# Kernel tuning notes

Measured on AMD Instinct MI355X. Metric: run time of the kernel, lower is better.

## Reference

```python
import jax, jax.numpy as jnp
import numpy as np

N = 50000
E = 800000
DIM_IN, DIM_H, DIM_OUT, HEADS = 128, 8, 32, 15
NEG_SLOPE = 0.2  # PyG GATv2Conv default


def gatv2_layer(x, src, dst, Wl, Wr, att, bias, num_nodes):
    """PyG GATv2Conv (share_weights=False, concat=True) with self-loops already in src/dst.
    x: [N, F_in]; Wl/Wr: [F_in, H*C]; att: [H, C]; bias: [H*C].
    """
    H, C = att.shape
    xl = (x @ Wl).reshape(-1, H, C)  # source transform [N,H,C]
    xr = (x @ Wr).reshape(-1, H, C)  # target transform [N,H,C]
    s = jax.nn.leaky_relu(xl[src] + xr[dst], negative_slope=NEG_SLOPE)  # [E,H,C]
    e = jnp.einsum('ehc,hc->eh', s, att)  # attention logits [E,H]
    # numerically-stable segment softmax over incoming edges of each dst node
    emax = jax.ops.segment_max(e, dst, num_segments=num_nodes)  # [N,H]
    ee = jnp.exp(e - emax[dst])
    denom = jax.ops.segment_sum(ee, dst, num_segments=num_nodes)  # [N,H]
    alpha = ee / denom[dst]  # self-loops guarantee denom > 0
    out = jax.ops.segment_sum(alpha[:, :, None] * xl[src], dst, num_segments=num_nodes)  # [N,H,C]
    return out.reshape(num_nodes, H * C) + bias


def setup_inputs() -> dict:
    key = jax.random.key(0)
    ks = jax.random.split(key, 10)
    x = jax.random.normal(ks[0], (N, DIM_IN), dtype=jnp.float32)
    edge_index = jax.random.randint(ks[1], (2, E), 0, N, dtype=jnp.int64)
    g1 = 1.0 / np.sqrt(DIM_IN)
    g2 = 1.0 / np.sqrt(DIM_H * HEADS)
    return {
        'x': x,
        'edge_index': edge_index,
        'W1l': jax.random.normal(ks[2], (DIM_IN, HEADS * DIM_H), dtype=jnp.float32) * g1,
        'W1r': jax.random.normal(ks[3], (DIM_IN, HEADS * DIM_H), dtype=jnp.float32) * g1,
        'att1': jax.random.normal(ks[4], (HEADS, DIM_H), dtype=jnp.float32) * (1.0 / np.sqrt(DIM_H)),
        'b1': jnp.zeros((HEADS * DIM_H,), dtype=jnp.float32),
        'W2l': jax.random.normal(ks[5], (HEADS * DIM_H, DIM_OUT), dtype=jnp.float32) * g2,
        'W2r': jax.random.normal(ks[6], (HEADS * DIM_H, DIM_OUT), dtype=jnp.float32) * g2,
        'att2': jax.random.normal(ks[7], (1, DIM_OUT), dtype=jnp.float32) * (1.0 / np.sqrt(DIM_OUT)),
        'b2': jnp.zeros((DIM_OUT,), dtype=jnp.float32),
    }


def reference(x, edge_index, W1l, W1r, att1, b1, W2l, W2r, att2, b2):
    n = x.shape[0]
    loops = jnp.arange(n, dtype=edge_index.dtype)
    src = jnp.concatenate([edge_index[0], loops])  # PyG add_self_loops=True
    dst = jnp.concatenate([edge_index[1], loops])
    h = gatv2_layer(x, src, dst, W1l, W1r, att1, b1, n)  # [N, HEADS*DIM_H]
    h = jax.nn.elu(h)
    # dropout(p=0.3) is identity in eval mode
    h = gatv2_layer(h, src, dst, W2l, W2r, att2, b2, n)  # heads=1 -> [N, DIM_OUT]
    return h, jax.nn.log_softmax(h, axis=1)
```

## Files before the change

### kernel.cpp

```cpp
#include <hip/hip_runtime.h>
#include <math.h>

namespace {
constexpr int NN  = 50000;
constexpr int EE  = 800000;
constexpr int FIN = 128;
constexpr int HC1 = 120;
constexpr int PAD = 128;
constexpr int F2  = 32;
constexpr int MT  = NN / 16;
constexpr int CAP = 64;
constexpr int NBIN = 64;
constexpr int BINW = 782;
constexpr int BINCAP = 16384;
constexpr int TILE = 4096;
constexpr int ABLK = (EE + TILE - 1) / TILE;
constexpr int CHUNKW = 12500;
constexpr int GB16 = (MT + 15) / 16;
constexpr int GB = (MT + 3) / 4;
constexpr float LOG2E = 1.442695041f;
}

typedef __attribute__((ext_vector_type(8))) short bf16x8;
typedef __attribute__((ext_vector_type(4))) float f32x4;
typedef __attribute__((ext_vector_type(2))) float f32x2;

template<int CTRL>
__device__ __forceinline__ float dppf(float x) {
    return __int_as_float(__builtin_amdgcn_mov_dpp(__float_as_int(x), CTRL, 0xF, 0xF, true));
}
__device__ __forceinline__ float quad_sum(float x) {
    x += dppf<0xB1>(x);
    x += dppf<0x4E>(x);
    return x;
}
__device__ __forceinline__ float rsum16(float x) {
    x += dppf<0x121>(x);
    x += dppf<0x122>(x);
    x += dppf<0x124>(x);
    x += dppf<0x128>(x);
    return x;
}
__device__ __forceinline__ float rmax16(float x) {
    x = fmaxf(x, dppf<0x121>(x));
    x = fmaxf(x, dppf<0x122>(x));
    x = fmaxf(x, dppf<0x124>(x));
    x = fmaxf(x, dppf<0x128>(x));
    return x;
}
template<int MASK>
__device__ __forceinline__ float swz_add(float x) {
    return x + __int_as_float(__builtin_amdgcn_ds_swizzle(__float_as_int(x), (MASK << 10) | 0x1F));
}

__device__ __forceinline__ unsigned short f2bf(float f) {
    unsigned int u = __float_as_uint(f);
    unsigned int r = (u + 0x7fffu + ((u >> 16) & 1u)) >> 16;
    return (unsigned short)r;
}
__device__ __forceinline__ f32x2 bf2v(unsigned int u) {
    f32x2 r;
    r.x = __uint_as_float(u << 16);
    r.y = __uint_as_float(u & 0xffff0000u);
    return r;
}
__device__ __forceinline__ f32x2 leaky2(f32x2 t) {
    return __builtin_elementwise_max(t, t * 0.2f);
}


__device__ void binA_body(int b, const unsigned int* __restrict__ raw,
                          int* __restrict__ cursor, unsigned int* __restrict__ binbuf) {
    __shared__ int lcnt[NBIN];
    __shared__ int lbase[NBIN];
    __shared__ int lcnt2[NBIN];
    __shared__ int is64_s;
    int tid = threadIdx.x;
    if (tid < NBIN) { lcnt[tid] = 0; lcnt2[tid] = 0; }
    if (tid < 64) {
        unsigned int hi = raw[2 * tid + 1];
        unsigned long long ball = __ballot(hi == 0u);
        if (tid == 0) is64_s = (ball == ~0ULL) ? 1 : 0;
    }
    __syncthreads();
    int is64 = is64_s;
    int e0 = b * TILE;
    #pragma unroll
    for (int i = 0; i < TILE / 256; ++i) {
        int e = e0 + i * 256 + tid;
        if (e < EE) {
            int d = is64 ? (int)raw[2 * (size_t)(EE + e)] : (int)raw[EE + e];
            atomicAdd(&lcnt[d / BINW], 1);
        }
    }
    __syncthreads();
    if (tid < NBIN) {
        int c = lcnt[tid];
        lbase[tid] = (c > 0) ? atomicAdd(&cursor[tid], c) : 0;
    }
    __syncthreads();
    #pragma unroll
    for (int i = 0; i < TILE / 256; ++i) {
        int e = e0 + i * 256 + tid;
        if (e < EE) {
            unsigned int s = is64 ? raw[2 * (size_t)e] : raw[e];
            unsigned int d = is64 ? raw[2 * (size_t)(EE + e)] : raw[EE + e];
            int bin = (int)d / BINW;
            int pos = lbase[bin] + atomicAdd(&lcnt2[bin], 1);
            if (pos < BINCAP) binbuf[(size_t)bin * BINCAP + pos] = (s << 16) | d;
        }
    }
}

__device__ void prep_body(int p, const float* __restrict__ W1l, const float* __restrict__ W1r,
                          const float* __restrict__ W2l, const float* __restrict__ W2r,
                          unsigned short* __restrict__ Bf1, unsigned short* __restrict__ Bf2) {
    int tid = p * 256 + threadIdx.x;
    if (tid < 4096) {
        int t = tid >> 8, lane = tid & 63;
        int kb = (tid >> 6) & 3;
        int k0 = kb * 32 + (lane >> 4) * 8;
        int n = (t & 7) * 16 + (lane & 15);
        const float* W = (t < 8) ? W1l : W1r;
        #pragma unroll
        for (int j = 0; j < 8; ++j)
            Bf1[(size_t)tid * 8 + j] = (n < HC1) ? f2bf(W[(k0 + j) * HC1 + n]) : (unsigned short)0;
    } else {
        int id = tid - 4096;
        int t = id >> 8, lane = id & 63;
        int kb = (id >> 6) & 3;
        int k0 = kb * 32 + (lane >> 4) * 8;
        int nl = (t & 1) * 16 + (lane & 15);
        const float* W = (t < 2) ? W2l : W2r;
        #pragma unroll
        for (int j = 0; j < 8; ++j) {
            int k = k0 + j;
            Bf2[(size_t)id * 8 + j] = (k < HC1) ? f2bf(W[k * F2 + nl]) : (unsigned short)0;
        }
    }
}

__global__ void __launch_bounds__(256) mergeA_kernel(
    const unsigned int* __restrict__ raw, int* __restrict__ cursor,
    unsigned int* __restrict__ binbuf,
    const float* __restrict__ W1l, const float* __restrict__ W1r,
    const float* __restrict__ W2l, const float* __restrict__ W2r,
    unsigned short* __restrict__ Bf1, unsigned short* __restrict__ Bf2) {
    if (blockIdx.x < ABLK) binA_body(blockIdx.x, raw, cursor, binbuf);
    else                   prep_body(blockIdx.x - ABLK, W1l, W1r, W2l, W2r, Bf1, Bf2);
}


__device__ void binB_body(int g, const int* __restrict__ cursor,
                          const unsigned int* __restrict__ binbuf,
                          int* __restrict__ cnt, unsigned short* __restrict__ bucket) {
    __shared__ int lc[BINW * 4];
    int tid = threadIdx.x;
    int ng0 = g * BINW;
    for (int i = tid; i < BINW * 4; i += 1024) lc[i] = 0;
    __syncthreads();
    int m = min(cursor[g], BINCAP);
    const unsigned int* bb = binbuf + (size_t)g * BINCAP;
    for (int i = tid; i < m; i += 1024) {
        unsigned int u = bb[i];
        int d = (int)(u & 0xffffu);
        int s = (int)(u >> 16);
        atomicAdd(&lc[(d - ng0) * 4 + s / CHUNKW], 1);
    }
    __syncthreads();
    if (tid < BINW) {
        int c0 = lc[tid * 4], c1 = lc[tid * 4 + 1], c2 = lc[tid * 4 + 2], c3 = lc[tid * 4 + 3];
        lc[tid * 4] = 0;
        lc[tid * 4 + 1] = c0;
        lc[tid * 4 + 2] = c0 + c1;
        lc[tid * 4 + 3] = c0 + c1 + c2;
        int n = ng0 + tid;
        if (n < NN) cnt[n] = min(c0 + c1 + c2 + c3, CAP);
    }
    __syncthreads();
    for (int i = tid; i < m; i += 1024) {
        unsigned int u = bb[i];
        int d = (int)(u & 0xffffu);
        int s = (int)(u >> 16);
        int pos = atomicAdd(&lc[(d - ng0) * 4 + s / CHUNKW], 1);
        if (pos < CAP) bucket[(size_t)d * CAP + pos] = (unsigned short)s;
    }
}

__device__ void gemm1_body(int g, const float* __restrict__ x,
                           const unsigned short* __restrict__ Bf,
                           unsigned short* __restrict__ xlb, unsigned short* __restrict__ xrb) {
    int wave = threadIdx.x >> 6, lane = threadIdx.x & 63;
    int mt = g * 16 + wave;
    if (mt >= MT) return;
    int n0 = mt * 16;
    int lr = lane & 15, kg = lane >> 4;
    const float* xrow = x + (size_t)(n0 + lr) * FIN + kg * 8;
    bf16x8 a[4];
    #pragma unroll
    for (int ko = 0; ko < 4; ++ko) {
        float4 lo = *(const float4*)(xrow + ko * 32);
        float4 hi = *(const float4*)(xrow + ko * 32 + 4);
        union { unsigned int u[4]; bf16x8 v; } cv;
        cv.u[0] = f2bf(lo.x) | ((unsigned int)f2bf(lo.y) << 16);
        cv.u[1] = f2bf(lo.z) | ((unsigned int)f2bf(lo.w) << 16);
        cv.u[2] = f2bf(hi.x) | ((unsigned int)f2bf(hi.y) << 16);
        cv.u[3] = f2bf(hi.z) | ((unsigned int)f2bf(hi.w) << 16);
        a[ko] = cv.v;
    }
    const bf16x8* bp = (const bf16x8*)Bf + lane;
    f32x4 acc[16];
    #pragma unroll
    for (int t = 0; t < 16; ++t) acc[t] = (f32x4){0.f, 0.f, 0.f, 0.f};
    #pragma unroll
    for (int t = 0; t < 16; ++t) {
        bf16x8 b0 = bp[(t * 4 + 0) * 64];
        bf16x8 b1 = bp[(t * 4 + 1) * 64];
        bf16x8 b2 = bp[(t * 4 + 2) * 64];
        bf16x8 b3 = bp[(t * 4 + 3) * 64];
        acc[t] = __builtin_amdgcn_mfma_f32_16x16x32_bf16(a[0], b0, acc[t], 0, 0, 0);
        acc[t] = __builtin_amdgcn_mfma_f32_16x16x32_bf16(a[1], b1, acc[t], 0, 0, 0);
        acc[t] = __builtin_amdgcn_mfma_f32_16x16x32_bf16(a[2], b2, acc[t], 0, 0, 0);
        acc[t] = __builtin_amdgcn_mfma_f32_16x16x32_bf16(a[3], b3, acc[t], 0, 0, 0);
    }
    #pragma unroll
    for (int t = 0; t < 16; ++t) {
        unsigned short* outp = (t < 8) ? xlb : xrb;
        int cg = (t & 7) * 16 + lr;
        #pragma unroll
        for (int r = 0; r < 4; ++r)
            outp[((size_t)(n0 + kg * 4 + r) << 7) + cg] = f2bf(acc[t][r]);
    }
}

__global__ void __launch_bounds__(1024) mergeB_kernel(
    const int* __restrict__ cursor, const unsigned int* __restrict__ binbuf,
    int* __restrict__ cnt, unsigned short* __restrict__ bucket,
    const float* __restrict__ x, const unsigned short* __restrict__ Bf,
    unsigned short* __restrict__ xlb, unsigned short* __restrict__ xrb) {
    if (blockIdx.x < NBIN) binB_body(blockIdx.x, cursor, binbuf, cnt, bucket);
    else                   gemm1_body(blockIdx.x - NBIN, x, Bf, xlb, xrb);
}

__global__ void __launch_bounds__(256) fused1_kernel(
    const unsigned short* __restrict__ bucket, const int* __restrict__ cnt,
    const unsigned short* __restrict__ xlb, const unsigned short* __restrict__ xrb,
    const float* __restrict__ att, const float* __restrict__ b1,
    unsigned int* __restrict__ hout) {
    int wave = threadIdx.x >> 6;
    int lane = threadIdx.x & 63;
    int n = blockIdx.x * 4 + wave;
    bool act = lane < 60;
    int ca = act ? 2 * lane : 0;
    const unsigned int* xl_u = (const unsigned int*)xlb;
    const unsigned int* xr_u = (const unsigned int*)xrb;
    f32x2 xrv = bf2v(xr_u[((size_t)n << 6) + lane]);
    float2 at = *(const float2*)(att + ca);
    float ax = at.x * LOG2E, ay = at.y * LOG2E;
    int deg = min(cnt[n], CAP);
    int mysrc = (lane < deg) ? (int)bucket[(size_t)n * CAP + lane] : 0;

    unsigned int A0=0,A1=0,A2=0,A3=0,B0=0,B1=0,B2=0,B3=0,
                 C0=0,C1=0,C2=0,C3=0,D0=0,D1=0,D2=0,D3=0;

#define LD4(U0,U1,U2,U3,J) { \
    U0 = xl_u[((unsigned)__builtin_amdgcn_readlane(mysrc,(J)+0) << 6) + lane]; \
    U1 = xl_u[((unsigned)__builtin_amdgcn_readlane(mysrc,(J)+1) << 6) + lane]; \
    U2 = xl_u[((unsigned)__builtin_amdgcn_readlane(mysrc,(J)+2) << 6) + lane]; \
    U3 = xl_u[((unsigned)__builtin_amdgcn_readlane(mysrc,(J)+3) << 6) + lane]; }

#define ED4(U0,U1,U2,U3,J) { \
    f32x2 r0 = bf2v(U0), r1 = bf2v(U1), r2 = bf2v(U2), r3 = bf2v(U3); \
    f32x2 t0 = leaky2(r0 + xrv), t1 = leaky2(r1 + xrv); \
    f32x2 t2 = leaky2(r2 + xrv), t3 = leaky2(r3 + xrv); \
    float p0 = quad_sum(fmaf(t0.y, ay, t0.x * ax)); \
    float p1 = quad_sum(fmaf(t1.y, ay, t1.x * ax)); \
    float p2 = quad_sum(fmaf(t2.y, ay, t2.x * ax)); \
    float p3 = quad_sum(fmaf(t3.y, ay, t3.x * ax)); \
    int nb = deg - (J); \
    float e0 = (nb > 0) ? exp2f(p0) : 0.f; \
    float e1 = (nb > 1) ? exp2f(p1) : 0.f; \
    float e2 = (nb > 2) ? exp2f(p2) : 0.f; \
    float e3 = (nb > 3) ? exp2f(p3) : 0.f; \
    s += (e0 + e1) + (e2 + e3); \
    o += r0 * e0; o += r1 * e1; o += r2 * e2; o += r3 * e3; }

    LD4(A0,A1,A2,A3, 0)
    if (deg > 4)  LD4(B0,B1,B2,B3, 4)
    if (deg > 8)  LD4(C0,C1,C2,C3, 8)

    float s;
    f32x2 o;
    {
        f32x2 r = bf2v(xl_u[((size_t)n << 6) + lane]);
        f32x2 t = leaky2(r + xrv);
        float p = quad_sum(fmaf(t.y, ay, t.x * ax));
        float e = exp2f(p);
        s = e; o = r * e;
    }
    #pragma unroll 1
    for (int base = 0; base < deg; base += 16) {
        if (deg > base + 12) LD4(D0,D1,D2,D3, base + 12)
        ED4(A0,A1,A2,A3, base + 0)
        if (deg > base + 16) LD4(A0,A1,A2,A3, base + 16)
        ED4(B0,B1,B2,B3, base + 4)
        if (deg > base + 20) LD4(B0,B1,B2,B3, base + 20)
        ED4(C0,C1,C2,C3, base + 8)
        if (deg > base + 24) LD4(C0,C1,C2,C3, base + 24)
        ED4(D0,D1,D2,D3, base + 12)
    }
#undef LD4
#undef ED4
    unsigned int packed = 0u;
    if (act) {
        float inv = 1.0f / s;
        float2 bv = *(const float2*)(b1 + ca);
        float v0 = o.x * inv + bv.x;
        float v1 = o.y * inv + bv.y;
        v0 = v0 > 0.f ? v0 : __expf(v0) - 1.f;
        v1 = v1 > 0.f ? v1 : __expf(v1) - 1.f;
        packed = (unsigned int)f2bf(v0) | ((unsigned int)f2bf(v1) << 16);
    }
    hout[(size_t)n * 64 + lane] = packed;
}

__global__ void __launch_bounds__(256) gemm2_mfma_kernel(
    const unsigned short* __restrict__ hb, const unsigned short* __restrict__ Bf,
    unsigned short* __restrict__ xl2b, unsigned short* __restrict__ xr2b) {
    int wave = threadIdx.x >> 6, lane = threadIdx.x & 63;
    int mt = blockIdx.x * 4 + wave;
    if (mt >= MT) return;
    int n0 = mt * 16;
    int lr = lane & 15, kg = lane >> 4;
    const unsigned short* ab = hb + (size_t)(n0 + lr) * FIN + kg * 8;
    bf16x8 a0 = *(const bf16x8*)(ab);
    bf16x8 a1 = *(const bf16x8*)(ab + 32);
    bf16x8 a2 = *(const bf16x8*)(ab + 64);
    bf16x8 a3 = *(const bf16x8*)(ab + 96);
    const bf16x8* bp = (const bf16x8*)Bf + lane;
    f32x4 acc[4];
    #pragma unroll
    for (int t = 0; t < 4; ++t) acc[t] = (f32x4){0.f, 0.f, 0.f, 0.f};
    #pragma unroll
    for (int t = 0; t < 4; ++t) {
        bf16x8 b0 = bp[(t * 4 + 0) * 64];
        bf16x8 b1 = bp[(t * 4 + 1) * 64];
        bf16x8 b2 = bp[(t * 4 + 2) * 64];
        bf16x8 b3 = bp[(t * 4 + 3) * 64];
        acc[t] = __builtin_amdgcn_mfma_f32_16x16x32_bf16(a0, b0, acc[t], 0, 0, 0);
        acc[t] = __builtin_amdgcn_mfma_f32_16x16x32_bf16(a1, b1, acc[t], 0, 0, 0);
        acc[t] = __builtin_amdgcn_mfma_f32_16x16x32_bf16(a2, b2, acc[t], 0, 0, 0);
        acc[t] = __builtin_amdgcn_mfma_f32_16x16x32_bf16(a3, b3, acc[t], 0, 0, 0);
    }
    #pragma unroll
    for (int t = 0; t < 4; ++t) {
        unsigned short* outp = (t < 2) ? xl2b : xr2b;
        int cg = (t & 1) * 16 + lr;
        #pragma unroll
        for (int r = 0; r < 4; ++r)
            outp[(size_t)(n0 + kg * 4 + r) * F2 + cg] = f2bf(acc[t][r]);
    }
}

__global__ void __launch_bounds__(256) fused2_kernel(
    const unsigned short* __restrict__ bucket, const int* __restrict__ cnt,
    const unsigned short* __restrict__ xl2b, const unsigned short* __restrict__ xr2b,
    const float* __restrict__ att2, const float* __restrict__ b2,
    float* __restrict__ out) {
    __shared__ int s_src[4][64];
    int wave = threadIdx.x >> 6;
    int lane = threadIdx.x & 63;
    int n = blockIdx.x * 4 + wave;
    int grp = lane >> 4;
    int cl = lane & 15;
    int c0 = 2 * cl;
    const unsigned int* xl_u = (const unsigned int*)xl2b;
    f32x2 xrv = bf2v(*(const unsigned int*)(xr2b + (size_t)n * F2 + c0));
    float2 at = *(const float2*)(att2 + c0);
    float ax = at.x * LOG2E, ay = at.y * LOG2E;
    int deg = min(cnt[n], CAP);
    s_src[wave][lane] = (lane < deg) ? (int)bucket[(size_t)n * CAP + lane] : 0;

    unsigned int uA = 0, uB = 0, uC = 0, uD = 0;
#define F2LD(U,I) U = xl_u[((unsigned)s_src[wave][4*(I)+grp] << 4) + cl];
#define F2ED(U,I) { \
    f32x2 r = bf2v(U); \
    f32x2 t = leaky2(r + xrv); \
    float p = rsum16(fmaf(t.y, ay, t.x * ax)); \
    float e = (4*(I)+grp < deg) ? exp2f(p) : 0.f; \
    s += e; o += r * e; }

    F2LD(uA, 0)
    if (deg > 4) F2LD(uB, 1)
    if (deg > 8) F2LD(uC, 2)

    float s;
    f32x2 o;
    {
        f32x2 r = bf2v(xl_u[((unsigned)n << 4) + cl]);
        f32x2 t = leaky2(r + xrv);
        float p = rsum16(fmaf(t.y, ay, t.x * ax));
        float e = (grp == 0) ? exp2f(p) : 0.f;
        s = e; o = r * e;
    }
    #pragma unroll 1
    for (int i0 = 0; 4 * i0 < deg; i0 += 4) {
        if (deg > 4*(i0+3)) F2LD(uD, i0+3)
        F2ED(uA, i0+0)
        if (deg > 4*(i0+4)) F2LD(uA, i0+4)
        F2ED(uB, i0+1)
        if (deg > 4*(i0+5)) F2LD(uB, i0+5)
        F2ED(uC, i0+2)
        if (deg > 4*(i0+6)) F2LD(uC, i0+6)
        F2ED(uD, i0+3)
    }
#undef F2LD
#undef F2ED
    s   = swz_add<16>(s);   s   += __shfl_xor(s, 32);
    o.x = swz_add<16>(o.x); o.x += __shfl_xor(o.x, 32);
    o.y = swz_add<16>(o.y); o.y += __shfl_xor(o.y, 32);
    float2 bv = *(const float2*)(b2 + c0);
    float inv = 1.0f / s;
    float v0 = o.x * inv + bv.x;
    float v1 = o.y * inv + bv.y;
    float mm = rmax16(fmaxf(v0, v1));
    float se = rsum16(__expf(v0 - mm) + __expf(v1 - mm));
    float lse = mm + __logf(se);
    if (lane < 16) {
        *(float2*)(out + (size_t)n * F2 + c0) = make_float2(v0, v1);
        *(float2*)(out + (size_t)NN * F2 + (size_t)n * F2 + c0) =
            make_float2(v0 - lse, v1 - lse);
    }
}

extern "C" void kernel_launch(void* const* d_in, const int* in_sizes, int n_in,
                              void* d_out, int out_size, void* d_ws, size_t ws_size,
                              hipStream_t stream) {
    const float* x    = (const float*)d_in[0];
    const unsigned int* ei_raw = (const unsigned int*)d_in[1];
    const float* W1l  = (const float*)d_in[2];
    const float* W1r  = (const float*)d_in[3];
    const float* att1 = (const float*)d_in[4];
    const float* b1   = (const float*)d_in[5];
    const float* W2l  = (const float*)d_in[6];
    const float* W2r  = (const float*)d_in[7];
    const float* att2 = (const float*)d_in[8];
    const float* b2   = (const float*)d_in[9];
    float* out = (float*)d_out;

    char* ws = (char*)d_ws;
    unsigned short* XL1b = (unsigned short*)ws; ws += (size_t)NN * PAD * 2;
    unsigned short* XR1b = (unsigned short*)ws; ws += (size_t)NN * PAD * 2;
    unsigned int* HHb    = (unsigned int*)ws;   ws += (size_t)NN * 64 * 4;
    unsigned short* XL2b = (unsigned short*)ws; ws += (size_t)NN * F2 * 2;
    unsigned short* XR2b = (unsigned short*)ws; ws += (size_t)NN * F2 * 2;
    unsigned short* BF1  = (unsigned short*)ws; ws += 16 * 4 * 64 * 8 * 2;
    unsigned short* BF2  = (unsigned short*)ws; ws += 4 * 4 * 64 * 8 * 2;
    unsigned short* BUCKET = (unsigned short*)ws; ws += (size_t)NN * CAP * 2;
    unsigned int* BINBUF = (unsigned int*)ws;   ws += (size_t)NBIN * BINCAP * 4;
    int* CURSOR = (int*)ws;                     ws += NBIN * 4;
    int* CNT    = (int*)ws;                     ws += (size_t)NN * 4;

    hipMemsetAsync(CURSOR, 0, NBIN * sizeof(int), stream);
    mergeA_kernel<<<ABLK + 20, 256, 0, stream>>>(ei_raw, CURSOR, BINBUF,
                                                 W1l, W1r, W2l, W2r, BF1, BF2);
    mergeB_kernel<<<NBIN + GB16, 1024, 0, stream>>>(CURSOR, BINBUF, CNT, BUCKET,
                                                    x, BF1, XL1b, XR1b);
    fused1_kernel<<<NN / 4, 256, 0, stream>>>(BUCKET, CNT, XL1b, XR1b, att1, b1, HHb);
    gemm2_mfma_kernel<<<GB, 256, 0, stream>>>((const unsigned short*)HHb, BF2, XL2b, XR2b);
    fused2_kernel<<<NN / 4, 256, 0, stream>>>(BUCKET, CNT, XL2b, XR2b, att2, b2, out);
}
```

Measured before the change: 226.4 us.

## Use persistent blocks with atomic work queues for both aggregation kernels

Replaces the one-wave-per-node grids of both aggregation kernels with 2048 persistent blocks. Each wave pulls node indices from one of eight atomic counters, with nodes partitioned into eight groups. The goal is to cut launch and tail overhead and to balance waves across nodes of varying degree. The layer-1 kernel also drops its software-pipelined 16-deep prefetch in favour of a simpler loop that loads 4 sources at a time through LDS. That loop may expose more gather latency, and the shared counters add atomic traffic.

Result: slower. 369.7 us (+63.3%).

```diff
diff --git a/kernel.cpp b/kernel.cpp
--- a/kernel.cpp
+++ b/kernel.cpp
@@ -18,6 +18,9 @@
 constexpr int CHUNKW = 12500;
 constexpr int GB16 = (MT + 15) / 16;
 constexpr int GB = (MT + 3) / 4;
+constexpr int NGRP = 8;
+constexpr int GRPN = NN / NGRP;
+constexpr int PBLK = 2048;
 constexpr float LOG2E = 1.442695041f;
 }
 
@@ -246,82 +249,84 @@
     const unsigned short* __restrict__ bucket, const int* __restrict__ cnt,
     const unsigned short* __restrict__ xlb, const unsigned short* __restrict__ xrb,
     const float* __restrict__ att, const float* __restrict__ b1,
-    unsigned int* __restrict__ hout) {
+    unsigned int* __restrict__ hout, int* __restrict__ qctr) {
+    __shared__ int s_src[4][64];
     int wave = threadIdx.x >> 6;
     int lane = threadIdx.x & 63;
-    int n = blockIdx.x * 4 + wave;
+    int grp = blockIdx.x & (NGRP - 1);
+    int* ctr = qctr + grp * 32;
+    int nbase = grp * GRPN;
     bool act = lane < 60;
     int ca = act ? 2 * lane : 0;
+    float2 at = *(const float2*)(att + ca);
+    float ax = at.x * LOG2E, ay = at.y * LOG2E;
     const unsigned int* xl_u = (const unsigned int*)xlb;
     const unsigned int* xr_u = (const unsigned int*)xrb;
-    f32x2 xrv = bf2v(xr_u[((size_t)n << 6) + lane]);
-    float2 at = *(const float2*)(att + ca);
-    float ax = at.x * LOG2E, ay = at.y * LOG2E;
-    int deg = min(cnt[n], CAP);
-    int mysrc = (lane < deg) ? (int)bucket[(size_t)n * CAP + lane] : 0;
-
-    unsigned int A0=0,A1=0,A2=0,A3=0,B0=0,B1=0,B2=0,B3=0,
-                 C0=0,C1=0,C2=0,C3=0,D0=0,D1=0,D2=0,D3=0;
-
-#define LD4(U0,U1,U2,U3,J) { \
-    U0 = xl_u[((unsigned)__builtin_amdgcn_readlane(mysrc,(J)+0) << 6) + lane]; \
-    U1 = xl_u[((unsigned)__builtin_amdgcn_readlane(mysrc,(J)+1) << 6) + lane]; \
-    U2 = xl_u[((unsigned)__builtin_amdgcn_readlane(mysrc,(J)+2) << 6) + lane]; \
-    U3 = xl_u[((unsigned)__builtin_amdgcn_readlane(mysrc,(J)+3) << 6) + lane]; }
-
-#define ED4(U0,U1,U2,U3,J) { \
-    f32x2 r0 = bf2v(U0), r1 = bf2v(U1), r2 = bf2v(U2), r3 = bf2v(U3); \
-    f32x2 t0 = leaky2(r0 + xrv), t1 = leaky2(r1 + xrv); \
-    f32x2 t2 = leaky2(r2 + xrv), t3 = leaky2(r3 + xrv); \
-    float p0 = quad_sum(fmaf(t0.y, ay, t0.x * ax)); \
-    float p1 = quad_sum(fmaf(t1.y, ay, t1.x * ax)); \
-    float p2 = quad_sum(fmaf(t2.y, ay, t2.x * ax)); \
-    float p3 = quad_sum(fmaf(t3.y, ay, t3.x * ax)); \
-    int nb = deg - (J); \
-    float e0 = (nb > 0) ? exp2f(p0) : 0.f; \
-    float e1 = (nb > 1) ? exp2f(p1) : 0.f; \
-    float e2 = (nb > 2) ? exp2f(p2) : 0.f; \
-    float e3 = (nb > 3) ? exp2f(p3) : 0.f; \
-    s += (e0 + e1) + (e2 + e3); \
-    o += r0 * e0; o += r1 * e1; o += r2 * e2; o += r3 * e3; }
-
-    LD4(A0,A1,A2,A3, 0)
-    if (deg > 4)  LD4(B0,B1,B2,B3, 4)
-    if (deg > 8)  LD4(C0,C1,C2,C3, 8)
-
-    float s;
-    f32x2 o;
-    {
-        f32x2 r = bf2v(xl_u[((size_t)n << 6) + lane]);
-        f32x2 t = leaky2(r + xrv);
-        float p = quad_sum(fmaf(t.y, ay, t.x * ax));
-        float e = exp2f(p);
-        s = e; o = r * e;
-    }
-    #pragma unroll 1
-    for (int base = 0; base < deg; base += 16) {
-        if (deg > base + 12) LD4(D0,D1,D2,D3, base + 12)
-        ED4(A0,A1,A2,A3, base + 0)
-        if (deg > base + 16) LD4(A0,A1,A2,A3, base + 16)
-        ED4(B0,B1,B2,B3, base + 4)
-        if (deg > base + 20) LD4(B0,B1,B2,B3, base + 20)
-        ED4(C0,C1,C2,C3, base + 8)
-        if (deg > base + 24) LD4(C0,C1,C2,C3, base + 24)
-        ED4(D0,D1,D2,D3, base + 12)
-    }
-#undef LD4
-#undef ED4
-    unsigned int packed = 0u;
-    if (act) {
-        float inv = 1.0f / s;
-        float2 bv = *(const float2*)(b1 + ca);
-        float v0 = o.x * inv + bv.x;
-        float v1 = o.y * inv + bv.y;
-        v0 = v0 > 0.f ? v0 : __expf(v0) - 1.f;
-        v1 = v1 > 0.f ? v1 : __expf(v1) - 1.f;
-        packed = (unsigned int)f2bf(v0) | ((unsigned int)f2bf(v1) << 16);
-    }
-    hout[(size_t)n * 64 + lane] = packed;
+
+    int t = 0;
+    if (lane == 0) t = atomicAdd(ctr, 1);
+    t = __shfl(t, 0);
+    while (t < GRPN) {
+        int tn = 0;
+        if (lane == 0) tn = atomicAdd(ctr, 1);
+        int n = nbase + t;
+
+        f32x2 xrv = bf2v(xr_u[((size_t)n << 6) + lane]);
+        int deg = min(cnt[n], CAP);
+        s_src[wave][lane] = (lane < deg) ? (int)bucket[(size_t)n * CAP + lane] : 0;
+        float s;
+        f32x2 o;
+        {
+            f32x2 r = bf2v(xl_u[((size_t)n << 6) + lane]);
+            f32x2 tt = leaky2(r + xrv);
+            float p = quad_sum(fmaf(tt.y, ay, tt.x * ax));
+            float e = exp2f(p);
+            s = e; o = r * e;
+        }
+        for (int j = 0; j < deg; j += 4) {
+            int4 ss = *(const int4*)&s_src[wave][j];
+            int s0 = __builtin_amdgcn_readfirstlane(ss.x);
+            int s1 = __builtin_amdgcn_readfirstlane(ss.y);
+            int s2 = __builtin_amdgcn_readfirstlane(ss.z);
+            int s3 = __builtin_amdgcn_readfirstlane(ss.w);
+            unsigned int u0 = xl_u[((size_t)(unsigned)s0 << 6) + lane];
+            unsigned int u1 = xl_u[((size_t)(unsigned)s1 << 6) + lane];
+            unsigned int u2 = xl_u[((size_t)(unsigned)s2 << 6) + lane];
+            unsigned int u3 = xl_u[((size_t)(unsigned)s3 << 6) + lane];
+            f32x2 r0 = bf2v(u0), r1 = bf2v(u1), r2 = bf2v(u2), r3 = bf2v(u3);
+            f32x2 t0 = leaky2(r0 + xrv);
+            f32x2 t1 = leaky2(r1 + xrv);
+            f32x2 t2 = leaky2(r2 + xrv);
+            f32x2 t3 = leaky2(r3 + xrv);
+            float p0 = quad_sum(fmaf(t0.y, ay, t0.x * ax));
+            float p1 = quad_sum(fmaf(t1.y, ay, t1.x * ax));
+            float p2 = quad_sum(fmaf(t2.y, ay, t2.x * ax));
+            float p3 = quad_sum(fmaf(t3.y, ay, t3.x * ax));
+            int nb = deg - j;
+            float e0 = exp2f(p0);
+            float e1 = (nb > 1) ? exp2f(p1) : 0.f;
+            float e2 = (nb > 2) ? exp2f(p2) : 0.f;
+            float e3 = (nb > 3) ? exp2f(p3) : 0.f;
+            s += (e0 + e1) + (e2 + e3);
+            o += r0 * e0;
+            o += r1 * e1;
+            o += r2 * e2;
+            o += r3 * e3;
+        }
+        unsigned int packed = 0u;
+        if (act) {
+            float inv = 1.0f / s;
+            float2 bv = *(const float2*)(b1 + ca);
+            float v0 = o.x * inv + bv.x;
+            float v1 = o.y * inv + bv.y;
+            v0 = v0 > 0.f ? v0 : __expf(v0) - 1.f;
+            v1 = v1 > 0.f ? v1 : __expf(v1) - 1.f;
+            packed = (unsigned int)f2bf(v0) | ((unsigned int)f2bf(v1) << 16);
+        }
+        hout[(size_t)n * 64 + lane] = packed;
+
+        t = __shfl(tn, 0);
+    }
 }
 
 __global__ void __launch_bounds__(256) gemm2_mfma_kernel(
@@ -366,70 +371,84 @@
     const unsigned short* __restrict__ bucket, const int* __restrict__ cnt,
     const unsigned short* __restrict__ xl2b, const unsigned short* __restrict__ xr2b,
     const float* __restrict__ att2, const float* __restrict__ b2,
-    float* __restrict__ out) {
+    float* __restrict__ out, int* __restrict__ qctr) {
     __shared__ int s_src[4][64];
     int wave = threadIdx.x >> 6;
     int lane = threadIdx.x & 63;
-    int n = blockIdx.x * 4 + wave;
-    int grp = lane >> 4;
+    int grp4 = lane >> 4;
     int cl = lane & 15;
     int c0 = 2 * cl;
+    int qg = blockIdx.x & (NGRP - 1);
+    int* ctr = qctr + qg * 32;
+    int nbase = qg * GRPN;
     const unsigned int* xl_u = (const unsigned int*)xl2b;
-    f32x2 xrv = bf2v(*(const unsigned int*)(xr2b + (size_t)n * F2 + c0));
     float2 at = *(const float2*)(att2 + c0);
     float ax = at.x * LOG2E, ay = at.y * LOG2E;
-    int deg = min(cnt[n], CAP);
-    s_src[wave][lane] = (lane < deg) ? (int)bucket[(size_t)n * CAP + lane] : 0;
-
-    unsigned int uA = 0, uB = 0, uC = 0, uD = 0;
-#define F2LD(U,I) U = xl_u[((unsigned)s_src[wave][4*(I)+grp] << 4) + cl];
+    float2 bv = *(const float2*)(b2 + c0);
+
+    int t = 0;
+    if (lane == 0) t = atomicAdd(ctr, 1);
+    t = __shfl(t, 0);
+    while (t < GRPN) {
+        int tn = 0;
+        if (lane == 0) tn = atomicAdd(ctr, 1);
+        int n = nbase + t;
+
+        f32x2 xrv = bf2v(*(const unsigned int*)(xr2b + (size_t)n * F2 + c0));
+        int deg = min(cnt[n], CAP);
+        s_src[wave][lane] = (lane < deg) ? (int)bucket[(size_t)n * CAP + lane] : 0;
+
+        unsigned int uA = 0, uB = 0, uC = 0, uD = 0;
+#define F2LD(U,I) U = xl_u[((unsigned)s_src[wave][4*(I)+grp4] << 4) + cl];
 #define F2ED(U,I) { \
-    f32x2 r = bf2v(U); \
-    f32x2 t = leaky2(r + xrv); \
-    float p = rsum16(fmaf(t.y, ay, t.x * ax)); \
-    float e = (4*(I)+grp < deg) ? exp2f(p) : 0.f; \
-    s += e; o += r * e; }
-
-    F2LD(uA, 0)
-    if (deg > 4) F2LD(uB, 1)
-    if (deg > 8) F2LD(uC, 2)
-
-    float s;
-    f32x2 o;
-    {
-        f32x2 r = bf2v(xl_u[((unsigned)n << 4) + cl]);
-        f32x2 t = leaky2(r + xrv);
-        float p = rsum16(fmaf(t.y, ay, t.x * ax));
-        float e = (grp == 0) ? exp2f(p) : 0.f;
-        s = e; o = r * e;
-    }
-    #pragma unroll 1
-    for (int i0 = 0; 4 * i0 < deg; i0 += 4) {
-        if (deg > 4*(i0+3)) F2LD(uD, i0+3)
-        F2ED(uA, i0+0)
-        if (deg > 4*(i0+4)) F2LD(uA, i0+4)
-        F2ED(uB, i0+1)
-        if (deg > 4*(i0+5)) F2LD(uB, i0+5)
-        F2ED(uC, i0+2)
-        if (deg > 4*(i0+6)) F2LD(uC, i0+6)
-        F2ED(uD, i0+3)
-    }
+        f32x2 r = bf2v(U); \
+        f32x2 tt = leaky2(r + xrv); \
+        float p = rsum16(fmaf(tt.y, ay, tt.x * ax)); \
+        float e = (4*(I)+grp4 < deg) ? exp2f(p) : 0.f; \
+        s += e; o += r * e; }
+
+        F2LD(uA, 0)
+        if (deg > 4) F2LD(uB, 1)
+        if (deg > 8) F2LD(uC, 2)
+
+        float s;
+        f32x2 o;
+        {
+            f32x2 r = bf2v(xl_u[((unsigned)n << 4) + cl]);
+            f32x2 tt = leaky2(r + xrv);
+            float p = rsum16(fmaf(tt.y, ay, tt.x * ax));
+            float e = (grp4 == 0) ? exp2f(p) : 0.f;
+            s = e; o = r * e;
+        }
+        #pragma unroll 1
+        for (int i0 = 0; 4 * i0 < deg; i0 += 4) {
+            if (deg > 4*(i0+3)) F2LD(uD, i0+3)
+            F2ED(uA, i0+0)
+            if (deg > 4*(i0+4)) F2LD(uA, i0+4)
+            F2ED(uB, i0+1)
+            if (deg > 4*(i0+5)) F2LD(uB, i0+5)
+            F2ED(uC, i0+2)
+            if (deg > 4*(i0+6)) F2LD(uC, i0+6)
+            F2ED(uD, i0+3)
+        }
 #undef F2LD
 #undef F2ED
-    s   = swz_add<16>(s);   s   += __shfl_xor(s, 32);
-    o.x = swz_add<16>(o.x); o.x += __shfl_xor(o.x, 32);
-    o.y = swz_add<16>(o.y); o.y += __shfl_xor(o.y, 32);
-    float2 bv = *(const float2*)(b2 + c0);
-    float inv = 1.0f / s;
-    float v0 = o.x * inv + bv.x;
-    float v1 = o.y * inv + bv.y;
-    float mm = rmax16(fmaxf(v0, v1));
-    float se = rsum16(__expf(v0 - mm) + __expf(v1 - mm));
-    float lse = mm + __logf(se);
-    if (lane < 16) {
-        *(float2*)(out + (size_t)n * F2 + c0) = make_float2(v0, v1);
-        *(float2*)(out + (size_t)NN * F2 + (size_t)n * F2 + c0) =
-            make_float2(v0 - lse, v1 - lse);
+        s   = swz_add<16>(s);   s   += __shfl_xor(s, 32);
+        o.x = swz_add<16>(o.x); o.x += __shfl_xor(o.x, 32);
+        o.y = swz_add<16>(o.y); o.y += __shfl_xor(o.y, 32);
+        float inv = 1.0f / s;
+        float v0 = o.x * inv + bv.x;
+        float v1 = o.y * inv + bv.y;
+        float mm = rmax16(fmaxf(v0, v1));
+        float se = rsum16(__expf(v0 - mm) + __expf(v1 - mm));
+        float lse = mm + __logf(se);
+        if (lane < 16) {
+            *(float2*)(out + (size_t)n * F2 + c0) = make_float2(v0, v1);
+            *(float2*)(out + (size_t)NN * F2 + (size_t)n * F2 + c0) =
+                make_float2(v0 - lse, v1 - lse);
+        }
+
+        t = __shfl(tn, 0);
     }
 }
 
@@ -459,14 +478,16 @@
     unsigned short* BUCKET = (unsigned short*)ws; ws += (size_t)NN * CAP * 2;
     unsigned int* BINBUF = (unsigned int*)ws;   ws += (size_t)NBIN * BINCAP * 4;
     int* CURSOR = (int*)ws;                     ws += NBIN * 4;
+    int* QC1    = (int*)ws;                     ws += NGRP * 32 * 4;
+    int* QC2    = (int*)ws;                     ws += NGRP * 32 * 4;
     int* CNT    = (int*)ws;                     ws += (size_t)NN * 4;
 
-    hipMemsetAsync(CURSOR, 0, NBIN * sizeof(int), stream);
+    hipMemsetAsync(CURSOR, 0, (NBIN + 2 * NGRP * 32) * sizeof(int), stream);
     mergeA_kernel<<<ABLK + 20, 256, 0, stream>>>(ei_raw, CURSOR, BINBUF,
                                                  W1l, W1r, W2l, W2r, BF1, BF2);
     mergeB_kernel<<<NBIN + GB16, 1024, 0, stream>>>(CURSOR, BINBUF, CNT, BUCKET,
                                                     x, BF1, XL1b, XR1b);
-    fused1_kernel<<<NN / 4, 256, 0, stream>>>(BUCKET, CNT, XL1b, XR1b, att1, b1, HHb);
+    fused1_kernel<<<PBLK, 256, 0, stream>>>(BUCKET, CNT, XL1b, XR1b, att1, b1, HHb, QC1);
     gemm2_mfma_kernel<<<GB, 256, 0, stream>>>((const unsigned short*)HHb, BF2, XL2b, XR2b);
-    fused2_kernel<<<NN / 4, 256, 0, stream>>>(BUCKET, CNT, XL2b, XR2b, att2, b2, out);
-}
+    fused2_kernel<<<PBLK, 256, 0, stream>>>(BUCKET, CNT, XL2b, XR2b, att2, b2, out, QC2);
+}
```
